# Kernel tuning notes

Measured on AMD Instinct MI355X. Metric: run time of the kernel, lower is better.

The kernel has to match this reference:

```python
import jax, jax.numpy as jnp
import numpy as np

N = 8192          # num_people
H = 128           # hidden_dim
ZE = 64           # zone_embed_dim
TE = 32           # temporal_embed_dim
NZ = 100          # num_zones
GRU_IN = H + ZE + TE


def _lin(k, out_d, in_d):
    kw, kb = jax.random.split(k)
    bound = 1.0 / np.sqrt(in_d)
    W = jax.random.uniform(kw, (out_d, in_d), minval=-bound, maxval=bound, dtype=jnp.float32)
    b = jax.random.uniform(kb, (out_d,), minval=-bound, maxval=bound, dtype=jnp.float32)
    return W, b


def setup_inputs() -> dict:
    key = jax.random.key(0)
    ks = jax.random.split(key, 12)
    t = jax.random.uniform(ks[0], (1,), dtype=jnp.float32)
    person_h = jax.random.normal(ks[1], (N, H), dtype=jnp.float32)
    gnn_zone_embeds = jax.random.normal(ks[2], (NZ, ZE), dtype=jnp.float32)
    W_time, b_time = _lin(ks[3], TE, 1)
    W_loc, b_loc = _lin(ks[4], NZ, H)
    Wq, bq = _lin(ks[5], H, H)
    Wk, bk = _lin(ks[6], H, H)
    Wv, bv = _lin(ks[7], H, H)
    W_merge, b_merge = _lin(ks[8], H, 2 * H)
    W_ih, b_ih = _lin(ks[9], 3 * H, GRU_IN)
    W_hh, b_hh = _lin(ks[10], 3 * H, H)
    ln_gamma = jnp.ones((H,), jnp.float32)
    ln_beta = jnp.zeros((H,), jnp.float32)
    return dict(t=t, person_h=person_h, gnn_zone_embeds=gnn_zone_embeds,
                W_time=W_time, b_time=b_time, W_loc=W_loc, b_loc=b_loc,
                Wq=Wq, bq=bq, Wk=Wk, bk=bk, Wv=Wv, bv=bv,
                W_merge=W_merge, b_merge=b_merge,
                W_ih=W_ih, b_ih=b_ih, W_hh=W_hh, b_hh=b_hh,
                ln_gamma=ln_gamma, ln_beta=ln_beta)


def reference(t, person_h, gnn_zone_embeds, W_time, b_time, W_loc, b_loc,
              Wq, bq, Wk, bk, Wv, bv, W_merge, b_merge,
              W_ih, b_ih, W_hh, b_hh, ln_gamma, ln_beta):
    n = person_h.shape[0]
    # spatial context: soft location distribution over zones
    loc_probs = jax.nn.softmax(person_h @ W_loc.T + b_loc, axis=-1)   # [N, NZ]
    spatial_context = loc_probs @ gnn_zone_embeds                     # [N, ZE]
    # leave-one-out social attention == full attention with diagonal masked
    q = person_h @ Wq.T + bq                                          # [N, H]
    k = person_h @ Wk.T + bk
    v = person_h @ Wv.T + bv
    scores = (q @ k.T) / np.sqrt(H).astype(np.float32)                # [N, N]
    diag = jnp.eye(n, dtype=bool)
    scores = jnp.where(diag, -jnp.inf, scores)
    attn = jax.nn.softmax(scores, axis=-1)
    social_context = attn @ v                                         # [N, H]
    h_interacted = jnp.concatenate([person_h, social_context], axis=-1) @ W_merge.T + b_merge
    time_context = jnp.broadcast_to(t.reshape(1, 1), (n, 1)) @ W_time.T + b_time  # [N, TE]
    gru_input = jnp.concatenate([h_interacted, spatial_context, time_context], axis=-1)
    # torch.nn.GRUCell: gates order (reset, update, new)
    gx = gru_input @ W_ih.T + b_ih                                    # [N, 3H]
    gh = person_h @ W_hh.T + b_hh
    xr, xz, xn = jnp.split(gx, 3, axis=-1)
    hr, hz, hn = jnp.split(gh, 3, axis=-1)
    r = jax.nn.sigmoid(xr + hr)
    z = jax.nn.sigmoid(xz + hz)
    ng = jnp.tanh(xn + r * hn)
    h_new = (1.0 - z) * ng + z * person_h
    d = h_new - person_h
    mu = jnp.mean(d, axis=-1, keepdims=True)
    var = jnp.var(d, axis=-1, keepdims=True)
    d = (d - mu) * jax.lax.rsqrt(var + 1e-5) * ln_gamma + ln_beta
    return d
```

## Files before the change

kernel.cpp:

```cpp
#include <hip/hip_runtime.h>


typedef __attribute__((ext_vector_type(8)))  short bf16x8;
typedef __attribute__((ext_vector_type(4)))  float f32x4;
typedef __attribute__((ext_vector_type(16))) float f32x16;
typedef __attribute__((ext_vector_type(4)))  unsigned uint4v;

#define N_P   8192
#define H_D   128
#define NCHNK 8
#define CHLEN (N_P / NCHNK)
#define KVB   64
#define NTIL  (CHLEN / KVB)
#define LDE   384

#if __has_builtin(__builtin_amdgcn_exp2f)
#define EXP2(x) __builtin_amdgcn_exp2f(x)
#else
#define EXP2(x) exp2f(x)
#endif

__device__ __forceinline__ short f2bf(float f) {
  unsigned u = __float_as_uint(f);
  u = (u + 0x7fffu + ((u >> 16) & 1u)) >> 16;
  return (short)u;
}
__device__ __forceinline__ float bf2f(short s) {
  return __uint_as_float(((unsigned)(unsigned short)s) << 16);
}
__device__ __forceinline__ unsigned pack2bf(float a, float b) {
  return (unsigned)(unsigned short)f2bf(a) | ((unsigned)(unsigned short)f2bf(b) << 16);
}

__device__ __forceinline__ int swzb(int row, int slot, int nslots) {
  return (row * nslots + (slot ^ (row & ((nslots - 1) & 7)))) << 4;
}

__device__ __forceinline__ unsigned cvtpk(float a, float b) {
  unsigned d;
  asm("v_cvt_pk_bf16_f32 %0, %1, %2" : "=v"(d) : "v"(a), "v"(b));
  return d;
}

__device__ __forceinline__ void swap32(unsigned& a, unsigned& b) {
#if __has_builtin(__builtin_amdgcn_permlane32_swap)
  auto r = __builtin_amdgcn_permlane32_swap(a, b, false, false);
  a = r[0]; b = r[1];
#else
  asm volatile("v_permlane32_swap_b32 %0, %1" : "+v"(a), "+v"(b));
#endif
}

typedef __attribute__((address_space(1))) const void GV;
typedef __attribute__((address_space(3))) void LV;
__device__ __forceinline__ void gld_lds16(const void* g, void* l) {
  __builtin_amdgcn_global_load_lds((GV*)g, (LV*)l, 16, 0, 0);
}

__constant__ const float QSCALE = 0.12751551485988857f;
#define LOG2E 1.4426950408889634f

__global__ __launch_bounds__(256) void init_kernel(
    const float* t, const float* W_time, const float* b_time,
    const float* W_loc, const float* b_loc,
    const float* Wq, const float* bq, const float* Wk, const float* bk,
    const float* Wv, const float* bv,
    const float* W_merge, const float* b_merge,
    const float* W_ih, const float* b_ih,
    const float* W_hh, const float* b_hh,
    const float* ph,
    short* W1, float* bias1, short* W_big, float* bias_big, short* PH2e) {
  const int b = blockIdx.x, tidl = threadIdx.x;
  if (b < 64) {
    int tid = b * 256 + tidl, stride = 64 * 256;
    for (int i = tid; i < 512 * 128; i += stride) {
      int r = i >> 7, k = i & 127;
      float v;
      if (r < 128)      v = Wq[r * 128 + k];
      else if (r < 256) v = Wk[(r - 128) * 128 + k];
      else if (r < 384) v = Wv[(r - 256) * 128 + k];
      else if (r < 484) v = W_loc[(r - 384) * 128 + k];
      else              v = 0.f;
      W1[i] = f2bf(v);
    }
    for (int i = tid; i < 512; i += stride) {
      float v;
      if (i < 128)      v = bq[i];
      else if (i < 256) v = bk[i - 128];
      else if (i < 384) v = bv[i - 256];
      else if (i < 484) v = b_loc[i - 384];
      else              v = 0.f;
      bias1[i] = v;
    }
  } else if (b < 576) {
    __shared__ float rowj[128];
    const int n = b - 64;
    if (tidl < 128) rowj[tidl] = (n < 384) ? W_ih[n * 224 + tidl] : 0.f;
    __syncthreads();
    {
      float acc = 0.f;
      if (n < 384) {
#pragma unroll 8
        for (int j = 0; j < 128; ++j) acc += rowj[j] * W_merge[j * 256 + tidl];
      }
      if (tidl < 128) {
        if (n < 256)      acc += W_hh[n * 128 + tidl];
        else if (n >= 384) acc = W_hh[(n - 128) * 128 + tidl];
      }
      W_big[n * 384 + tidl] = f2bf(acc);
    }
    if (tidl < 128) {
      int k2 = 256 + tidl;
      float v = 0.f;
      if (n < 384) {
        if (k2 < 320)      v = W_ih[n * 224 + 128 + (k2 - 256)];
        else if (k2 < 352) v = W_ih[n * 224 + 192 + (k2 - 320)];
      }
      W_big[n * 384 + k2] = f2bf(v);
    }
    if (tidl < 64) {
      float p = rowj[tidl] * b_merge[tidl] + rowj[tidl + 64] * b_merge[tidl + 64];
#pragma unroll
      for (int mk = 1; mk < 64; mk <<= 1) p += __shfl_xor(p, mk);
      if (tidl == 0) {
        float bb;
        if (n < 256)      bb = b_ih[n] + p + b_hh[n];
        else if (n < 384) bb = b_ih[n] + p;
        else              bb = b_hh[n - 128];
        bias_big[n] = bb;
      }
    }
  } else {
    int tid = (b - 576) * 256 + tidl, stride = 128 * 256;
    for (int i = tid; i < N_P * 16; i += stride) {
      int r = i >> 4, d8 = (i & 15) * 8;
      float4 a  = *(const float4*)(ph + (size_t)r * 128 + d8);
      float4 a2 = *(const float4*)(ph + (size_t)r * 128 + d8 + 4);
      int4 o;
      o.x = (int)pack2bf(a.x,  a.y);
      o.y = (int)pack2bf(a.z,  a.w);
      o.z = (int)pack2bf(a2.x, a2.y);
      o.w = (int)pack2bf(a2.z, a2.w);
      *(int4*)(PH2e + (size_t)r * LDE + d8) = o;
    }
    const float t0 = t[0];
    for (int i = tid; i < N_P * 8; i += stride) {
      int r = i >> 3, j8 = (i & 7) * 8;
      float v[8];
#pragma unroll
      for (int k = 0; k < 8; ++k) {
        int j = j8 + k;
        v[k] = (j < 32) ? (t0 * W_time[j] + b_time[j]) : 0.f;
      }
      int4 o;
      o.x = (int)pack2bf(v[0], v[1]);
      o.y = (int)pack2bf(v[2], v[3]);
      o.z = (int)pack2bf(v[4], v[5]);
      o.w = (int)pack2bf(v[6], v[7]);
      *(int4*)(PH2e + (size_t)r * LDE + 320 + j8) = o;
    }
  }
}

template <int MODE, int K>
__global__ __launch_bounds__(256, 3) void gemm64_kernel(
    const short* __restrict__ X, int ldx, const short* __restrict__ W,
    const float* __restrict__ bias,
    short* out_q, short* out_k, short* out_vT, float* out_loc,
    short* out_gx) {
  __shared__ short Xl[64 * 128];
  __shared__ short Wl[128 * 128];
  const int tid = threadIdx.x;
  const int lin = blockIdx.y * 128 + blockIdx.x;
  const int xcd = lin & 7, j = lin >> 3;
  const int bmIdx = xcd * 16 + (j & 15);
  const int bnIdx = j >> 4;
  const int bm = bmIdx * 64, bn = bnIdx * 128;
  const int l = tid & 63, wid = tid >> 6;
  const int g = l >> 4, c = l & 15;
  const int wr = wid >> 1, wc = wid & 1;
  f32x4 acc[2][4] = {};
  constexpr int KT = K / 128;
#pragma unroll 1
  for (int kt = 0; kt < KT; ++kt) {
    const int k0 = kt * 128;
#pragma unroll
    for (int pass = 0; pass < 4; ++pass) {
      int s = tid + pass * 256;
      int row = s >> 4, p = s & 15;
      int lsl = p ^ (row & 7);
      gld_lds16(X + (size_t)(bm + row) * ldx + k0 + lsl * 8, (char*)Xl + s * 16);
    }
#pragma unroll
    for (int pass = 0; pass < 8; ++pass) {
      int s = tid + pass * 256;
      int row = s >> 4, p = s & 15;
      int lsl = p ^ (row & 7);
      gld_lds16(W + (size_t)(bn + row) * K + k0 + lsl * 8, (char*)Wl + s * 16);
    }
    __syncthreads();
#pragma unroll
    for (int kc = 0; kc < 4; ++kc) {
      bf16x8 a[2], bfr[4];
#pragma unroll
      for (int mi = 0; mi < 2; ++mi)
        a[mi] = *(const bf16x8*)((const char*)Xl + swzb(wr * 32 + mi * 16 + c, kc * 4 + g, 16));
#pragma unroll
      for (int ni = 0; ni < 4; ++ni)
        bfr[ni] = *(const bf16x8*)((const char*)Wl + swzb(wc * 64 + ni * 16 + c, kc * 4 + g, 16));
#pragma unroll
      for (int mi = 0; mi < 2; ++mi)
#pragma unroll
        for (int ni = 0; ni < 4; ++ni)
          acc[mi][ni] = __builtin_amdgcn_mfma_f32_16x16x32_bf16(a[mi], bfr[ni], acc[mi][ni], 0, 0, 0);
    }
    if (kt + 1 < KT) __syncthreads();
  }
  if constexpr (MODE == 0) {
    if (bnIdx == 2) {
      __syncthreads();
      short* T = Wl;
#pragma unroll
      for (int mi = 0; mi < 2; ++mi)
#pragma unroll
        for (int ni = 0; ni < 4; ++ni)
#pragma unroll
          for (int r = 0; r < 4; ++r) {
            int rl = wr * 32 + mi * 16 + 4 * g + r;
            int cl = wc * 64 + ni * 16 + c;
            T[rl * 130 + cl] = f2bf(acc[mi][ni][r] + bias[256 + cl]);
          }
      __syncthreads();
#pragma unroll
      for (int pass = 0; pass < 32; ++pass) {
        int d = pass * 4 + (tid >> 6);
        int jj = tid & 63;
        out_vT[(size_t)d * N_P + bm + jj] = T[jj * 130 + d];
      }
    } else {
#pragma unroll
      for (int mi = 0; mi < 2; ++mi)
#pragma unroll
        for (int ni = 0; ni < 4; ++ni)
#pragma unroll
          for (int r = 0; r < 4; ++r) {
            int row = bm + wr * 32 + mi * 16 + 4 * g + r;
            int col = bn + wc * 64 + ni * 16 + c;
            float val = acc[mi][ni][r] + bias[col];
            if (col < 128)      out_q[row * 128 + col] = f2bf(val * QSCALE);
            else if (col < 256) out_k[row * 128 + col - 128] = f2bf(val);
            else if (col >= 384 && col < 484) out_loc[row * 112 + col - 384] = val;
          }
    }
  } else {
#pragma unroll
    for (int mi = 0; mi < 2; ++mi)
#pragma unroll
      for (int ni = 0; ni < 4; ++ni)
#pragma unroll
        for (int r = 0; r < 4; ++r) {
          int row = bm + wr * 32 + mi * 16 + 4 * g + r;
          int col = bn + wc * 64 + ni * 16 + c;
          out_gx[row * 512 + col] = f2bf(acc[mi][ni][r] + bias[col]);
        }
  }
}

__global__ __launch_bounds__(256, 2) void attn_kernel(
    const short* __restrict__ qb, const short* __restrict__ kb,
    const short* __restrict__ vT, short* __restrict__ pacc,
    float* __restrict__ pml) {
  __shared__ short Kl[2][KVB * H_D];
  __shared__ short Vl[2][H_D * KVB];
  const int tid = threadIdx.x;
  const int qbk = blockIdx.x >> 3, ch = blockIdx.x & 7;
  const int chbase = ch * CHLEN;
  const int l = tid & 63, wid = tid >> 6;
  const int c32 = l & 31, hi = l >> 5;
  const int qrow0w = qbk * 128 + wid * 32;

  char* ldsK = (char*)&Kl[0][0];
  char* ldsV = (char*)&Vl[0][0];

  auto stage = [&](int b, int tt) {
    const int off = tt * KVB;
#pragma unroll
    for (int j = 0; j < 4; ++j) {
      const int i = tid + j * 256;
      const int kr = i >> 4, ks = (i & 15) ^ (kr & 15);
      gld_lds16(kb + (size_t)(chbase + off + kr) * 128 + ks * 8,
                ldsK + b * 16384 + i * 16);
      const int vr = i >> 3, vs = (i & 7) ^ (vr & 7);
      gld_lds16(vT + (size_t)vr * N_P + chbase + off + vs * 8,
                ldsV + b * 16384 + i * 16);
    }
  };

  bf16x8 qf[8];
#pragma unroll
  for (int sl = 0; sl < 8; ++sl)
    qf[sl] = *(const bf16x8*)(qb + (size_t)(qrow0w + c32) * 128 + sl * 16 + hi * 8);

  bf16x8 ones;
#pragma unroll
  for (int j = 0; j < 8; ++j) ones[j] = (short)0x3F80;

  const int c15 = c32 & 15;
  const int kbase0 = c32 * 256;
  int koff[8];
#pragma unroll
  for (int sl = 0; sl < 8; ++sl) koff[sl] = ((2 * sl + hi) ^ c15) << 4;
  const int xh = (c32 >> 1) & 3, x0 = c32 & 1;
  const int xb = (hi ^ x0) << 4;
  int voff[4], vbase[4];
#pragma unroll
  for (int s4 = 0; s4 < 4; ++s4) voff[s4] = (s4 ^ xh) << 5;
#pragma unroll
  for (int db = 0; db < 4; ++db) vbase[db] = (db * 32 + c32) * 128 + xb;

  f32x16 acc[4] = {};
  f32x16 accl = {};
  float m = -1e30f;

  stage(0, 0);
  asm volatile("s_waitcnt vmcnt(0)" ::: "memory");
  __builtin_amdgcn_s_barrier();
  int cur = 0;

#pragma unroll 1
  for (int t = 0; t < NTIL; ++t) {
    if (t + 1 < NTIL) stage(cur ^ 1, t + 1);

    const int kv0 = chbase + t * KVB;
    const char* Kb = (const char*)&Kl[cur][0];
    const char* Vb = (const char*)&Vl[cur][0];

    f32x16 s0 = {}, s1 = {};
    __builtin_amdgcn_s_setprio(1);
#pragma unroll
    for (int sl = 0; sl < 8; ++sl) {
      bf16x8 k0 = *(const bf16x8*)(Kb + kbase0 + koff[sl]);
      bf16x8 k1 = *(const bf16x8*)(Kb + kbase0 + 8192 + koff[sl]);
      s0 = __builtin_amdgcn_mfma_f32_32x32x16_bf16(k0, qf[sl], s0, 0, 0, 0);
      s1 = __builtin_amdgcn_mfma_f32_32x32x16_bf16(k1, qf[sl], s1, 0, 0, 0);
    }
    __builtin_amdgcn_s_setprio(0);

    if (qrow0w + 32 > kv0 && qrow0w < kv0 + 64) {
      const int qr = qrow0w + c32;
#pragma unroll
      for (int r = 0; r < 16; ++r) {
        const int rowp = (r & 3) + 8 * (r >> 2) + 4 * hi;
        s0[r] = (kv0 + rowp == qr) ? -1e30f : s0[r];
        s1[r] = (kv0 + 32 + rowp == qr) ? -1e30f : s1[r];
      }
    }

    if (t == 0) {
      f32x16 mx;
#pragma unroll
      for (int r = 0; r < 16; ++r) mx[r] = fmaxf(s0[r], s1[r]);
#pragma unroll
      for (int w2 = 8; w2 >= 1; w2 >>= 1)
#pragma unroll
        for (int r = 0; r < w2; ++r) mx[r] = fmaxf(mx[r], mx[r + w2]);
      m = fmaxf(mx[0], __shfl_xor(mx[0], 32));
    }

#pragma unroll
    for (int r = 0; r < 16; ++r) s0[r] = EXP2(s0[r] - m);
#pragma unroll
    for (int r = 0; r < 16; ++r) s1[r] = EXP2(s1[r] - m);

    auto pvslice = [&](const f32x16& ss, int base, int sl4) {
      unsigned dA = cvtpk(ss[base + 0], ss[base + 1]);
      unsigned dB = cvtpk(ss[base + 2], ss[base + 3]);
      unsigned dC = cvtpk(ss[base + 4], ss[base + 5]);
      unsigned dD = cvtpk(ss[base + 6], ss[base + 7]);
      swap32(dA, dC);
      swap32(dB, dD);
      uint4v w = {dA, dB, dC, dD};
      bf16x8 pa = __builtin_bit_cast(bf16x8, w);
#pragma unroll
      for (int db = 0; db < 4; ++db) {
        bf16x8 vfr = *(const bf16x8*)(Vb + vbase[db] + voff[sl4]);
        acc[db] = __builtin_amdgcn_mfma_f32_32x32x16_bf16(pa, vfr, acc[db], 0, 0, 0);
      }
      accl = __builtin_amdgcn_mfma_f32_32x32x16_bf16(pa, ones, accl, 0, 0, 0);
    };
    __builtin_amdgcn_s_setprio(1);
    pvslice(s0, 0, 0);
    pvslice(s0, 8, 1);
    pvslice(s1, 0, 2);
    pvslice(s1, 8, 3);
    __builtin_amdgcn_s_setprio(0);

    if (t + 1 < NTIL) {
      asm volatile("s_waitcnt vmcnt(0)" ::: "memory");
      __builtin_amdgcn_s_barrier();
      asm volatile("" ::: "memory");
    }
    cur ^= 1;
  }

#pragma unroll
  for (int db = 0; db < 4; ++db)
#pragma unroll
    for (int r = 0; r < 16; ++r) {
      const int qr = qrow0w + (r & 3) + 8 * (r >> 2) + 4 * hi;
      pacc[((size_t)ch * N_P + qr) * 128 + db * 32 + c32] = f2bf(acc[db][r]);
    }
  {
    const int rr = (c32 & 3) | (((c32 >> 3) & 3) << 2);
    float own = (((c32 >> 2) & 1) == hi) ? accl[rr] : 0.f;
    float lv = own + __shfl_xor(own, 32);
    if (hi == 0) {
      const int qr = qrow0w + c32;
      pml[((size_t)ch * N_P + qr) * 2]     = m;
      pml[((size_t)ch * N_P + qr) * 2 + 1] = lv;
    }
  }
}

__global__ __launch_bounds__(256) void combine_spatial_kernel(
    const short* __restrict__ pacc, const float* __restrict__ pml,
    const float* __restrict__ locf, const float* __restrict__ E,
    short* __restrict__ PH2e) {
  const int b = blockIdx.x, tid = threadIdx.x;
  if (b < 2048) {
    const int sub = tid >> 6;
    const int t6 = tid & 63;
    const int row = b * 4 + sub;
    const int d0 = 2 * t6;
    float mv[NCHNK], lv[NCHNK], M = -1e30f;
#pragma unroll
    for (int cc = 0; cc < NCHNK; ++cc) {
      float2 ml = *(const float2*)(pml + ((size_t)cc * N_P + row) * 2);
      mv[cc] = ml.x; lv[cc] = ml.y;
      M = fmaxf(M, mv[cc]);
    }
    float L = 0.f, Ox = 0.f, Oy = 0.f;
#pragma unroll
    for (int cc = 0; cc < NCHNK; ++cc) {
      unsigned pp = *(const unsigned*)(pacc + ((size_t)cc * N_P + row) * 128 + d0);
      float w = EXP2(mv[cc] - M);
      L += lv[cc] * w;
      Ox += bf2f((short)(pp & 0xffffu)) * w;
      Oy += bf2f((short)(pp >> 16)) * w;
    }
    float inv = 1.f / L;
    *(unsigned*)(PH2e + (size_t)row * LDE + 128 + d0) = pack2bf(Ox * inv, Oy * inv);
  } else {
    __shared__ float pl[4][104];
    int wid = tid >> 6, l = tid & 63;
    int row = (b - 2048) * 4 + wid;
    float v0 = locf[row * 112 + l];
    float v1 = (l + 64 < 100) ? locf[row * 112 + 64 + l] : -1e30f;
    float m = fmaxf(v0, v1);
#pragma unroll
    for (int mk = 1; mk < 64; mk <<= 1) m = fmaxf(m, __shfl_xor(m, mk));
    float p0 = EXP2((v0 - m) * LOG2E);
    float p1 = (l + 64 < 100) ? EXP2((v1 - m) * LOG2E) : 0.f;
    float s = p0 + p1;
#pragma unroll
    for (int mk = 1; mk < 64; mk <<= 1) s += __shfl_xor(s, mk);
    float inv = 1.f / s;
    pl[wid][l] = p0 * inv;
    if (l + 64 < 100) pl[wid][64 + l] = p1 * inv;
    float acc = 0.f;
#pragma unroll 4
    for (int z = 0; z < 100; ++z) acc += pl[wid][z] * E[z * 64 + l];
    PH2e[row * LDE + 256 + l] = f2bf(acc);
  }
}

__global__ __launch_bounds__(256) void final_kernel(const short* __restrict__ gxs,
                                                    const float* __restrict__ ph,
                                                    const float* __restrict__ gamma,
                                                    const float* __restrict__ beta,
                                                    float* __restrict__ out) {
  int tid = threadIdx.x, wid = tid >> 6, l = tid & 63;
  int row = blockIdx.x * 4 + wid;
  const int d0 = 2 * l;
  const short* gr = gxs + (size_t)row * 512 + d0;
  unsigned usr = *(const unsigned*)(gr);
  unsigned usz = *(const unsigned*)(gr + 128);
  unsigned uxn = *(const unsigned*)(gr + 256);
  unsigned uhn = *(const unsigned*)(gr + 384);
  float2 hh = *(const float2*)(ph + (size_t)row * 128 + d0);
  float dd[2];
#pragma unroll
  for (int j = 0; j < 2; ++j) {
    float sr = bf2f((short)(j ? (usr >> 16) : (usr & 0xffffu)));
    float sz = bf2f((short)(j ? (usz >> 16) : (usz & 0xffffu)));
    float xn = bf2f((short)(j ? (uxn >> 16) : (uxn & 0xffffu)));
    float hn = bf2f((short)(j ? (uhn >> 16) : (uhn & 0xffffu)));
    float h = j ? hh.y : hh.x;
    float r = 1.f / (1.f + EXP2(-LOG2E * sr));
    float z = 1.f / (1.f + EXP2(-LOG2E * sz));
    float a = xn + r * hn;
    float ng = 1.f - 2.f / (1.f + EXP2(2.f * LOG2E * a));
    dd[j] = (1.f - z) * (ng - h);
  }
  float s = dd[0] + dd[1], ss = dd[0] * dd[0] + dd[1] * dd[1];
#pragma unroll
  for (int mk = 1; mk < 64; mk <<= 1) {
    s += __shfl_xor(s, mk);
    ss += __shfl_xor(ss, mk);
  }
  float mu = s * (1.f / 128.f);
  float var = ss * (1.f / 128.f) - mu * mu;
  float rs = rsqrtf(var + 1e-5f);
  float2 gm = *(const float2*)(gamma + d0);
  float2 bt = *(const float2*)(beta + d0);
  float2 o;
  o.x = (dd[0] - mu) * rs * gm.x + bt.x;
  o.y = (dd[1] - mu) * rs * gm.y + bt.y;
  *(float2*)(out + (size_t)row * 128 + d0) = o;
}

extern "C" void kernel_launch(void* const* d_in, const int* in_sizes, int n_in,
                              void* d_out, int out_size, void* d_ws, size_t ws_size,
                              hipStream_t stream) {
  const float* t       = (const float*)d_in[0];
  const float* ph      = (const float*)d_in[1];
  const float* E       = (const float*)d_in[2];
  const float* W_time  = (const float*)d_in[3];
  const float* b_time  = (const float*)d_in[4];
  const float* W_loc   = (const float*)d_in[5];
  const float* b_loc   = (const float*)d_in[6];
  const float* Wq      = (const float*)d_in[7];
  const float* bq      = (const float*)d_in[8];
  const float* Wk      = (const float*)d_in[9];
  const float* bk      = (const float*)d_in[10];
  const float* Wv      = (const float*)d_in[11];
  const float* bv      = (const float*)d_in[12];
  const float* W_merge = (const float*)d_in[13];
  const float* b_merge = (const float*)d_in[14];
  const float* W_ih    = (const float*)d_in[15];
  const float* b_ih    = (const float*)d_in[16];
  const float* W_hh    = (const float*)d_in[17];
  const float* b_hh    = (const float*)d_in[18];
  const float* gamma   = (const float*)d_in[19];
  const float* beta    = (const float*)d_in[20];
  float* out = (float*)d_out;

  char* w = (char*)d_ws;
  auto alloc = [&](size_t bytes) {
    char* p = w;
    w += (bytes + 255) & ~(size_t)255;
    return p;
  };
  short* W1      = (short*)alloc(512 * 128 * 2);
  float* bias1   = (float*)alloc(512 * 4);
  short* W_big   = (short*)alloc(512 * 384 * 2);
  float* bias_big= (float*)alloc(512 * 4);
  short* PH2e    = (short*)alloc((size_t)N_P * LDE * 2);
  short* qbuf    = (short*)alloc((size_t)N_P * 128 * 2);
  short* kbuf    = (short*)alloc((size_t)N_P * 128 * 2);
  short* vT      = (short*)alloc((size_t)128 * N_P * 2);
  float* locf    = (float*)alloc((size_t)N_P * 112 * 4);
  short* gxs     = (short*)alloc((size_t)N_P * 512 * 2);
  short* pacc    = (short*)alloc((size_t)NCHNK * N_P * 128 * 2);
  float* pml     = (float*)alloc((size_t)NCHNK * N_P * 2 * 4);

  init_kernel<<<704, 256, 0, stream>>>(t, W_time, b_time, W_loc, b_loc, Wq, bq,
                                       Wk, bk, Wv, bv, W_merge, b_merge,
                                       W_ih, b_ih, W_hh, b_hh, ph,
                                       W1, bias1, W_big, bias_big, PH2e);
  gemm64_kernel<0, 128><<<dim3(128, 4), 256, 0, stream>>>(
      PH2e, LDE, W1, bias1, qbuf, kbuf, vT, locf, nullptr);
  attn_kernel<<<512, 256, 0, stream>>>(qbuf, kbuf, vT, pacc, pml);
  combine_spatial_kernel<<<4096, 256, 0, stream>>>(pacc, pml, locf, E, PH2e);
  gemm64_kernel<2, 384><<<dim3(128, 4), 256, 0, stream>>>(
      PH2e, LDE, W_big, bias_big, nullptr, nullptr, nullptr, nullptr, gxs);
  final_kernel<<<2048, 256, 0, stream>>>(gxs, ph, gamma, beta, out);
}
```

Baseline: 88.31 us.

## Split attention KV into 12 chunks with 32-wide tiles and VALU row sums

The attention kernel now splits keys into 12 uneven chunks of 21–22 tiles each and halves the KV tile to 32 rows. This gives 768 blocks at 3 blocks per CU (half the LDS per block) instead of 512 at 2, to spread work across the GPU more evenly. The row-sum MFMA against a ones vector is replaced with a per-lane VALU sum of the fp32 probabilities, which frees MFMA issue slots. In exchange, each block passes through more barriers and staging rounds, the partial buffers and combine step carry more chunks, and the denominator now uses fp32 values rather than the bf16-rounded ones.

```diff
diff --git a/kernel.cpp b/kernel.cpp
--- a/kernel.cpp
+++ b/kernel.cpp
@@ -8,10 +8,8 @@
 
 #define N_P   8192
 #define H_D   128
-#define NCHNK 8
-#define CHLEN (N_P / NCHNK)
-#define KVB   64
-#define NTIL  (CHLEN / KVB)
+#define NCHNK 12
+#define KVB   32
 #define LDE   384
 
 #if __has_builtin(__builtin_amdgcn_exp2f)
@@ -266,15 +264,17 @@
   }
 }
 
-__global__ __launch_bounds__(256, 2) void attn_kernel(
+__global__ __launch_bounds__(256, 3) void attn_kernel(
     const short* __restrict__ qb, const short* __restrict__ kb,
     const short* __restrict__ vT, short* __restrict__ pacc,
     float* __restrict__ pml) {
   __shared__ short Kl[2][KVB * H_D];
   __shared__ short Vl[2][H_D * KVB];
   const int tid = threadIdx.x;
-  const int qbk = blockIdx.x >> 3, ch = blockIdx.x & 7;
-  const int chbase = ch * CHLEN;
+  const int qbk = blockIdx.x / NCHNK, ch = blockIdx.x % NCHNK;
+  const int tile0 = (ch < 4) ? ch * 22 : 88 + (ch - 4) * 21;
+  const int nt = (ch < 4) ? 22 : 21;
+  const int chbase = tile0 * KVB;
   const int l = tid & 63, wid = tid >> 6;
   const int c32 = l & 31, hi = l >> 5;
   const int qrow0w = qbk * 128 + wid * 32;
@@ -283,16 +283,16 @@
   char* ldsV = (char*)&Vl[0][0];
 
   auto stage = [&](int b, int tt) {
-    const int off = tt * KVB;
-#pragma unroll
-    for (int j = 0; j < 4; ++j) {
+    const int off = (tile0 + tt) * KVB;
+#pragma unroll
+    for (int j = 0; j < 2; ++j) {
       const int i = tid + j * 256;
       const int kr = i >> 4, ks = (i & 15) ^ (kr & 15);
-      gld_lds16(kb + (size_t)(chbase + off + kr) * 128 + ks * 8,
-                ldsK + b * 16384 + i * 16);
-      const int vr = i >> 3, vs = (i & 7) ^ (vr & 7);
-      gld_lds16(vT + (size_t)vr * N_P + chbase + off + vs * 8,
-                ldsV + b * 16384 + i * 16);
+      gld_lds16(kb + (size_t)(off + kr) * 128 + ks * 8,
+                ldsK + b * 8192 + i * 16);
+      const int vr = i >> 2, vs = (i & 3) ^ (vr & 3);
+      gld_lds16(vT + (size_t)vr * N_P + off + vs * 8,
+                ldsV + b * 8192 + i * 16);
     }
   };
 
@@ -300,27 +300,21 @@
 #pragma unroll
   for (int sl = 0; sl < 8; ++sl)
     qf[sl] = *(const bf16x8*)(qb + (size_t)(qrow0w + c32) * 128 + sl * 16 + hi * 8);
-
-  bf16x8 ones;
-#pragma unroll
-  for (int j = 0; j < 8; ++j) ones[j] = (short)0x3F80;
 
   const int c15 = c32 & 15;
   const int kbase0 = c32 * 256;
   int koff[8];
 #pragma unroll
   for (int sl = 0; sl < 8; ++sl) koff[sl] = ((2 * sl + hi) ^ c15) << 4;
-  const int xh = (c32 >> 1) & 3, x0 = c32 & 1;
-  const int xb = (hi ^ x0) << 4;
-  int voff[4], vbase[4];
-#pragma unroll
-  for (int s4 = 0; s4 < 4; ++s4) voff[s4] = (s4 ^ xh) << 5;
-#pragma unroll
-  for (int db = 0; db < 4; ++db) vbase[db] = (db * 32 + c32) * 128 + xb;
+  const int c3 = c32 & 3;
+  int voff[2], vbase[4];
+#pragma unroll
+  for (int s4 = 0; s4 < 2; ++s4) voff[s4] = ((2 * s4 + hi) ^ c3) << 4;
+#pragma unroll
+  for (int db = 0; db < 4; ++db) vbase[db] = (db * 32 + c32) * 64;
 
   f32x16 acc[4] = {};
-  f32x16 accl = {};
-  float m = -1e30f;
+  float m = -1e30f, lsum = 0.f;
 
   stage(0, 0);
   asm volatile("s_waitcnt vmcnt(0)" ::: "memory");
@@ -328,38 +322,33 @@
   int cur = 0;
 
 #pragma unroll 1
-  for (int t = 0; t < NTIL; ++t) {
-    if (t + 1 < NTIL) stage(cur ^ 1, t + 1);
+  for (int t = 0; t < nt; ++t) {
+    if (t + 1 < nt) stage(cur ^ 1, t + 1);
 
     const int kv0 = chbase + t * KVB;
-    const char* Kb = (const char*)&Kl[cur][0];
-    const char* Vb = (const char*)&Vl[cur][0];
-
-    f32x16 s0 = {}, s1 = {};
+    const char* Kb = ldsK + cur * 8192;
+    const char* Vb = ldsV + cur * 8192;
+
+    f32x16 s0 = {};
     __builtin_amdgcn_s_setprio(1);
 #pragma unroll
     for (int sl = 0; sl < 8; ++sl) {
       bf16x8 k0 = *(const bf16x8*)(Kb + kbase0 + koff[sl]);
-      bf16x8 k1 = *(const bf16x8*)(Kb + kbase0 + 8192 + koff[sl]);
       s0 = __builtin_amdgcn_mfma_f32_32x32x16_bf16(k0, qf[sl], s0, 0, 0, 0);
-      s1 = __builtin_amdgcn_mfma_f32_32x32x16_bf16(k1, qf[sl], s1, 0, 0, 0);
     }
     __builtin_amdgcn_s_setprio(0);
 
-    if (qrow0w + 32 > kv0 && qrow0w < kv0 + 64) {
+    if (qrow0w + 32 > kv0 && qrow0w < kv0 + KVB) {
       const int qr = qrow0w + c32;
 #pragma unroll
       for (int r = 0; r < 16; ++r) {
         const int rowp = (r & 3) + 8 * (r >> 2) + 4 * hi;
         s0[r] = (kv0 + rowp == qr) ? -1e30f : s0[r];
-        s1[r] = (kv0 + 32 + rowp == qr) ? -1e30f : s1[r];
       }
     }
 
     if (t == 0) {
-      f32x16 mx;
-#pragma unroll
-      for (int r = 0; r < 16; ++r) mx[r] = fmaxf(s0[r], s1[r]);
+      f32x16 mx = s0;
 #pragma unroll
       for (int w2 = 8; w2 >= 1; w2 >>= 1)
 #pragma unroll
@@ -369,8 +358,6 @@
 
 #pragma unroll
     for (int r = 0; r < 16; ++r) s0[r] = EXP2(s0[r] - m);
-#pragma unroll
-    for (int r = 0; r < 16; ++r) s1[r] = EXP2(s1[r] - m);
 
     auto pvslice = [&](const f32x16& ss, int base, int sl4) {
       unsigned dA = cvtpk(ss[base + 0], ss[base + 1]);
@@ -386,16 +373,15 @@
         bf16x8 vfr = *(const bf16x8*)(Vb + vbase[db] + voff[sl4]);
         acc[db] = __builtin_amdgcn_mfma_f32_32x32x16_bf16(pa, vfr, acc[db], 0, 0, 0);
       }
-      accl = __builtin_amdgcn_mfma_f32_32x32x16_bf16(pa, ones, accl, 0, 0, 0);
+#pragma unroll
+      for (int j = 0; j < 8; ++j) lsum += ss[base + j];
     };
     __builtin_amdgcn_s_setprio(1);
     pvslice(s0, 0, 0);
     pvslice(s0, 8, 1);
-    pvslice(s1, 0, 2);
-    pvslice(s1, 8, 3);
     __builtin_amdgcn_s_setprio(0);
 
-    if (t + 1 < NTIL) {
+    if (t + 1 < nt) {
       asm volatile("s_waitcnt vmcnt(0)" ::: "memory");
       __builtin_amdgcn_s_barrier();
       asm volatile("" ::: "memory");
@@ -411,9 +397,7 @@
       pacc[((size_t)ch * N_P + qr) * 128 + db * 32 + c32] = f2bf(acc[db][r]);
     }
   {
-    const int rr = (c32 & 3) | (((c32 >> 3) & 3) << 2);
-    float own = (((c32 >> 2) & 1) == hi) ? accl[rr] : 0.f;
-    float lv = own + __shfl_xor(own, 32);
+    float lv = lsum + __shfl_xor(lsum, 32);
     if (hi == 0) {
       const int qr = qrow0w + c32;
       pml[((size_t)ch * N_P + qr) * 2]     = m;
@@ -570,7 +554,7 @@
                                        W1, bias1, W_big, bias_big, PH2e);
   gemm64_kernel<0, 128><<<dim3(128, 4), 256, 0, stream>>>(
       PH2e, LDE, W1, bias1, qbuf, kbuf, vT, locf, nullptr);
-  attn_kernel<<<512, 256, 0, stream>>>(qbuf, kbuf, vT, pacc, pml);
+  attn_kernel<<<768, 256, 0, stream>>>(qbuf, kbuf, vT, pacc, pml);
   combine_spatial_kernel<<<4096, 256, 0, stream>>>(pacc, pml, locf, E, PH2e);
   gemm64_kernel<2, 384><<<dim3(128, 4), 256, 0, stream>>>(
       PH2e, LDE, W_big, bias_big, nullptr, nullptr, nullptr, nullptr, gxs);
```

Result: slower. 92.65 us (+4.9%).
